# Performance work log

Measured on AMD Instinct MI355X. Metric: run time of the kernel, lower is better.

The kernel has to match this reference:

```python
import jax, jax.numpy as jnp
import numpy as np

INF = 100000000.0
TOPK = 13
ALPHA = 1
BETA = 6


def box_cxcywh_to_xyxy(b):
    cx, cy, w, h = jnp.split(b, 4, axis=-1)
    return jnp.concatenate([cx - 0.5 * w, cy - 0.5 * h, cx + 0.5 * w, cy + 0.5 * h], axis=-1)


def generalized_box_iou(boxes1, boxes2):
    # boxes1: [N,4] xyxy, boxes2: [G,4] xyxy -> [N,G]
    area1 = (boxes1[:, 2] - boxes1[:, 0]) * (boxes1[:, 3] - boxes1[:, 1])
    area2 = (boxes2[:, 2] - boxes2[:, 0]) * (boxes2[:, 3] - boxes2[:, 1])
    lt = jnp.maximum(boxes1[:, None, :2], boxes2[None, :, :2])
    rb = jnp.minimum(boxes1[:, None, 2:], boxes2[None, :, 2:])
    wh = jnp.clip(rb - lt, 0.0)
    inter = wh[..., 0] * wh[..., 1]
    union = area1[:, None] + area2[None, :] - inter
    iou = inter / union
    lt_e = jnp.minimum(boxes1[:, None, :2], boxes2[None, :, :2])
    rb_e = jnp.maximum(boxes1[:, None, 2:], boxes2[None, :, 2:])
    wh_e = jnp.clip(rb_e - lt_e, 0.0)
    area_e = wh_e[..., 0] * wh_e[..., 1]
    return iou - (area_e - union) / area_e


def _assign_one(cls_logits, bbox_pred, gt_boxes, gt_labels):
    # cls_logits [N,C], bbox_pred [N,4] cxcywh, gt_boxes [G,4] cxcywh, gt_labels [G]
    N = bbox_pred.shape[0]
    G = gt_boxes.shape[0]
    scores = jax.nn.sigmoid(cls_logits)
    overlaps = -generalized_box_iou(box_cxcywh_to_xyxy(bbox_pred), box_cxcywh_to_xyxy(gt_boxes))  # [N,G]
    bbox_scores = scores[:, gt_labels]                       # [N,G] gather per-gt class score
    alignment = bbox_scores ** ALPHA * overlaps ** BETA      # [N,G]
    # per-gt topk over queries
    cand_metrics, cand_idxs = jax.lax.top_k(alignment.T, TOPK)  # [G,K]
    is_pos = cand_metrics > 0
    vals = jnp.take_along_axis(overlaps.T, cand_idxs, axis=1)   # [G,K]
    rows = jnp.broadcast_to(jnp.arange(G)[:, None], (G, TOPK))
    cols = jnp.where(is_pos, cand_idxs, N)  # out-of-bounds col -> dropped
    oinf = jnp.full((G, N), -INF, dtype=overlaps.dtype)
    oinf = oinf.at[rows, cols].set(vals, mode='drop')
    max_overlaps = oinf.max(axis=0)     # [N]
    argmax_overlaps = oinf.argmax(axis=0)
    pos = max_overlaps != -INF
    assigned_gt_inds = jnp.where(pos, argmax_overlaps + 1, 0)
    assign_metrics = jnp.where(pos, alignment[jnp.arange(N), argmax_overlaps], 0.0)
    assigned_labels = jnp.where(pos, gt_labels[argmax_overlaps], -1)
    return assigned_gt_inds, assigned_labels, assign_metrics


def setup_inputs() -> dict:
    key = jax.random.key(0)
    k1, k2, k3, k4 = jax.random.split(key, 4)
    bs, N, C, G = 16, 4000, 80, 300
    return {
        'pred_logits': jax.random.normal(k1, (bs, N, C), dtype=jnp.float32),
        'pred_boxes': jax.random.uniform(k2, (bs, N, 4), dtype=jnp.float32, minval=0.05, maxval=0.95),
        'gt_boxes': jax.random.uniform(k3, (bs, G, 4), dtype=jnp.float32, minval=0.05, maxval=0.95),
        'gt_labels': jax.random.randint(k4, (bs, G), 0, C),
    }


def reference(pred_logits, pred_boxes, gt_boxes, gt_labels):
    # Fixed-shape equivalent of matched_list: assigned_gt_inds[b,q] == 0 means
    # background; k>0 means query q matched to gt k-1 (same semantics as the
    # (valid_query_idx, valid_assigned_gt_inds) pairs in the torch code).
    return jax.vmap(_assign_one)(pred_logits, pred_boxes, gt_boxes, gt_labels)
```

## Files before the change

### kernel.cpp

```cpp
#include <hip/hip_runtime.h>

#define NPRED  4000
#define NGROUP 1000
#define NGT    300
#define NCLS   80
#define TOPKK  13
#define NCHUNK 125

typedef unsigned long long u64;

__device__ __forceinline__ float frcp(float x) { return __builtin_amdgcn_rcpf(x); }
__device__ __forceinline__ float fexp(float x) {
    return __builtin_amdgcn_exp2f(x * 1.44269504088896341f);
}

__device__ __forceinline__ float neg_giou_x(float4 p, float gx1, float gy1,
                                            float gx2, float gy2, float garea) {
    float pa  = (p.z - p.x) * (p.w - p.y);
    float whx = fmaxf(fminf(p.z, gx2) - fmaxf(p.x, gx1), 0.0f);
    float why = fmaxf(fminf(p.w, gy2) - fmaxf(p.y, gy1), 0.0f);
    float inter = whx * why;
    float uni = pa + garea - inter;
    float iou = inter * frcp(uni);
    float wex = fmaxf(p.z, gx2) - fminf(p.x, gx1);
    float wey = fmaxf(p.w, gy2) - fminf(p.y, gy1);
    float area_e = wex * wey;
    return (area_e - uni) * frcp(area_e) - iou;
}

__device__ __forceinline__ float4 to_xyxy(float4 pb) {
    return make_float4(pb.x - 0.5f * pb.z, pb.y - 0.5f * pb.w,
                       pb.x + 0.5f * pb.z, pb.y + 0.5f * pb.w);
}

__device__ __forceinline__ float sigmoid_fast(float x) {
    return frcp(1.0f + fexp(-x));
}

__device__ __forceinline__ float pow6(float x) {
    float x2 = x * x;
    float x4 = x2 * x2;
    return x2 * x4;
}

__device__ __forceinline__ unsigned ord_float(float f) {
    unsigned u = __float_as_uint(f);
    return u ^ ((unsigned)(((int)u) >> 31) | 0x80000000u);
}

__device__ __forceinline__ u64 pack_key(float v, int n) {
    return ((u64)__float_as_uint(v) << 32) | (u64)(~(unsigned)n);
}

__global__ void init_keys(u64* keys, int n) {
    int i = blockIdx.x * blockDim.x + threadIdx.x;
    if (i < n) keys[i] = 0ULL;
}

__global__ __launch_bounds__(256) void sig_transpose(const float* __restrict__ logits,
                                                     const float4* __restrict__ pboxes,
                                                     float* __restrict__ st,
                                                     float4* __restrict__ pxyxy,
                                                     u64* __restrict__ keys,
                                                     int total_keys) {
    const int tid = threadIdx.x;
    const int gid = blockIdx.x * 256 + tid;
    if (gid < total_keys) keys[gid] = 0ULL;

    const int b = blockIdx.x / NCHUNK;
    const int n0 = (blockIdx.x % NCHUNK) * 32;

    if (tid < 32) {
        pxyxy[(size_t)b * NPRED + n0 + tid] =
            to_xyxy(pboxes[(size_t)b * NPRED + n0 + tid]);
    }

    __shared__ float tile[NCLS][32 + 1];

    const float4* src = (const float4*)(logits + ((size_t)b * NPRED + n0) * NCLS);
    #pragma unroll
    for (int it = 0; it < 3; ++it) {
        int i4 = tid + it * 256;
        if (i4 < 640) {
            int p = i4 / 20;
            int c = (i4 - p * 20) * 4;
            float4 v = src[i4];
            tile[c + 0][p] = sigmoid_fast(v.x);
            tile[c + 1][p] = sigmoid_fast(v.y);
            tile[c + 2][p] = sigmoid_fast(v.z);
            tile[c + 3][p] = sigmoid_fast(v.w);
        }
    }
    __syncthreads();
    float* dstbase = st + (size_t)b * NCLS * NPRED + n0;
    #pragma unroll
    for (int it = 0; it < 3; ++it) {
        int w4 = tid + it * 256;
        if (w4 < 640) {
            int c = w4 >> 3, r4 = (w4 & 7) * 4;
            float4 v = make_float4(tile[c][r4], tile[c][r4 + 1],
                                   tile[c][r4 + 2], tile[c][r4 + 3]);
            *(float4*)(dstbase + (size_t)c * NPRED + r4) = v;
        }
    }
}

template <bool PRE>
__global__ __launch_bounds__(256) void topk_scatter(const float* __restrict__ logits,
                                                    const float* __restrict__ st,
                                                    const float4* __restrict__ pboxes,
                                                    const float4* __restrict__ pxyxy,
                                                    const float4* __restrict__ gboxes,
                                                    const int* __restrict__ glabels,
                                                    u64* __restrict__ keys) {
    const int blk = blockIdx.x;
    const int b = blk / NGT;
    const int g = blk - b * NGT;
    const int tid = threadIdx.x;
    const int wave = tid >> 6;
    const int lane = tid & 63;

    __shared__ __align__(16) float s_key[NPRED];
    __shared__ u64 s_wave[4];
    __shared__ u64 s_win[TOPKK];

    float4 gb = gboxes[b * NGT + g];
    const int lab = glabels[b * NGT + g];
    const float gx1 = gb.x - 0.5f * gb.z;
    const float gy1 = gb.y - 0.5f * gb.w;
    const float gx2 = gb.x + 0.5f * gb.z;
    const float gy2 = gb.y + 0.5f * gb.w;
    const float garea = (gx2 - gx1) * (gy2 - gy1);

    const float* lg = logits + (size_t)b * NPRED * NCLS + lab;
    const float* srow = st + ((size_t)b * NCLS + lab) * NPRED;
    const float4* srow4 = (const float4*)srow;
    const float4* pbb = pboxes + (size_t)b * NPRED;
    const float4* pxr = pxyxy + (size_t)b * NPRED;

    u64 b1 = 0ULL, b2 = 0ULL;
    #pragma unroll
    for (int j = 0; j < 4; ++j) {
        int grp = tid + j * 256;
        if (grp < NGROUP) {
            int n0 = grp * 4;
            float s0, s1, s2, s3;
            float4 p0, p1, p2, p3;
            if (PRE) {
                float4 s4 = srow4[grp];
                s0 = s4.x; s1 = s4.y; s2 = s4.z; s3 = s4.w;
                p0 = pxr[n0]; p1 = pxr[n0 + 1]; p2 = pxr[n0 + 2]; p3 = pxr[n0 + 3];
            } else {
                s0 = sigmoid_fast(lg[(size_t)(n0 + 0) * NCLS]);
                s1 = sigmoid_fast(lg[(size_t)(n0 + 1) * NCLS]);
                s2 = sigmoid_fast(lg[(size_t)(n0 + 2) * NCLS]);
                s3 = sigmoid_fast(lg[(size_t)(n0 + 3) * NCLS]);
                p0 = to_xyxy(pbb[n0]);     p1 = to_xyxy(pbb[n0 + 1]);
                p2 = to_xyxy(pbb[n0 + 2]); p3 = to_xyxy(pbb[n0 + 3]);
            }
            float v0 = s0 * pow6(neg_giou_x(p0, gx1, gy1, gx2, gy2, garea));
            float v1 = s1 * pow6(neg_giou_x(p1, gx1, gy1, gx2, gy2, garea));
            float v2 = s2 * pow6(neg_giou_x(p2, gx1, gy1, gx2, gy2, garea));
            float v3 = s3 * pow6(neg_giou_x(p3, gx1, gy1, gx2, gy2, garea));
            *(float4*)&s_key[n0] = make_float4(v0, v1, v2, v3);
            u64 k0 = pack_key(v0, n0);
            u64 k1 = pack_key(v1, n0 + 1);
            u64 k2 = pack_key(v2, n0 + 2);
            u64 k3 = pack_key(v3, n0 + 3);
            if (k0 > b1) { b2 = b1; b1 = k0; } else if (k0 > b2) b2 = k0;
            if (k1 > b1) { b2 = b1; b1 = k1; } else if (k1 > b2) b2 = k1;
            if (k2 > b1) { b2 = b1; b1 = k2; } else if (k2 > b2) b2 = k2;
            if (k3 > b1) { b2 = b1; b1 = k3; } else if (k3 > b2) b2 = k3;
        }
    }

    {
        u64 m1 = b1;
        #pragma unroll
        for (int m = 1; m < 64; m <<= 1) {
            u64 o = __shfl_xor(m1, m, 64);
            if (o > m1) m1 = o;
        }
        if (lane == 0) s_wave[wave] = m1;
    }

    int nwin = 0;
    for (int k = 0; k < TOPKK; ++k) {
        __syncthreads();
        u64 t1 = s_wave[0];
        u64 c;
        c = s_wave[1]; if (c > t1) t1 = c;
        c = s_wave[2]; if (c > t1) t1 = c;
        c = s_wave[3]; if (c > t1) t1 = c;
        if ((unsigned)(t1 >> 32) == 0u) break;
        if (tid == 0) s_win[k] = t1;
        nwin = k + 1;
        int n1 = (int)(~(unsigned)t1);
        int ownerTid = (n1 >> 2) & 255;
        if (tid == ownerTid) {
            s_key[n1] = 0.0f;
            if (b2 != 0ULL) { b1 = b2; b2 = 0ULL; }
            else {
                b1 = 0ULL;
                #pragma unroll
                for (int jj = 0; jj < 4; ++jj) {
                    int grp = tid + jj * 256;
                    if (grp >= NGROUP) continue;
                    int n0 = grp * 4;
                    float4 q = *(const float4*)&s_key[n0];
                    u64 c0 = pack_key(q.x, n0);
                    u64 c1 = pack_key(q.y, n0 + 1);
                    u64 c2 = pack_key(q.z, n0 + 2);
                    u64 c3 = pack_key(q.w, n0 + 3);
                    if (c0 > b1) { b2 = b1; b1 = c0; } else if (c0 > b2) b2 = c0;
                    if (c1 > b1) { b2 = b1; b1 = c1; } else if (c1 > b2) b2 = c1;
                    if (c2 > b1) { b2 = b1; b1 = c2; } else if (c2 > b2) b2 = c2;
                    if (c3 > b1) { b2 = b1; b1 = c3; } else if (c3 > b2) b2 = c3;
                }
            }
        }
        if ((ownerTid >> 6) == wave) {
            u64 m1 = b1;
            #pragma unroll
            for (int m = 1; m < 64; m <<= 1) {
                u64 o = __shfl_xor(m1, m, 64);
                if (o > m1) m1 = o;
            }
            if (lane == 0) s_wave[wave] = m1;
        }
    }
    __syncthreads();

    if (tid < nwin) {
        u64 t = s_win[tid];
        int wi = (int)(~(unsigned)t);
        float o;
        if (PRE) {
            o = neg_giou_x(pxr[wi], gx1, gy1, gx2, gy2, garea);
        } else {
            o = neg_giou_x(to_xyxy(pbb[wi]), gx1, gy1, gx2, gy2, garea);
        }
        unsigned mbits = (unsigned)(t >> 32) >> 16;
        u64 key = ((u64)ord_float(o) << 32)
                | ((u64)(511u - (unsigned)g) << 23)
                | ((u64)mbits << 7);
        atomicMax(&keys[(size_t)b * NPRED + wi], key);
    }
}

__global__ void finalize(const int* __restrict__ glabels,
                         const u64* __restrict__ keys,
                         float* __restrict__ out, int total) {
    int i = blockIdx.x * blockDim.x + threadIdx.x;
    if (i >= total) return;
    int b = i / NPRED;
    u64 key = keys[i];
    float o0 = 0.0f, o1 = -1.0f, o2 = 0.0f;
    if (key != 0ULL) {
        int g = 511 - (int)((key >> 23) & 0x1FF);
        o0 = (float)(g + 1);
        o1 = (float)glabels[b * NGT + g];
        o2 = __uint_as_float(((unsigned)(key >> 7) & 0xFFFFu) << 16);
    }
    out[i] = o0;
    out[(size_t)total + i] = o1;
    out[(size_t)2 * total + i] = o2;
}

extern "C" void kernel_launch(void* const* d_in, const int* in_sizes, int n_in,
                              void* d_out, int out_size, void* d_ws, size_t ws_size,
                              hipStream_t stream) {
    const float* logits  = (const float*)d_in[0];
    const float4* pboxes = (const float4*)d_in[1];
    const float4* gboxes = (const float4*)d_in[2];
    const int* glabels   = (const int*)d_in[3];

    const int bs = in_sizes[3] / NGT;
    const int total = bs * NPRED;
    char* ws = (char*)d_ws;
    u64* keys   = (u64*)ws;                    ws += (size_t)total * 8;
    float* st   = (float*)ws;                  ws += (size_t)bs * NCLS * NPRED * 4;
    float4* pxy = (float4*)ws;                 ws += (size_t)total * 16;
    float* out = (float*)d_out;

    const size_t need = (size_t)(ws - (char*)d_ws);
    if (ws_size >= need) {
        sig_transpose<<<bs * NCHUNK, 256, 0, stream>>>(logits, pboxes, st, pxy,
                                                       keys, total);
        topk_scatter<true><<<bs * NGT, 256, 0, stream>>>(logits, st, pboxes, pxy,
                                                         gboxes, glabels, keys);
    } else {
        init_keys<<<(total + 255) / 256, 256, 0, stream>>>(keys, total);
        topk_scatter<false><<<bs * NGT, 256, 0, stream>>>(logits, st, pboxes, pxy,
                                                          gboxes, glabels, keys);
    }
    finalize<<<(total + 255) / 256, 256, 0, stream>>>(glabels, keys, out, total);
}
```

Baseline: 124.1 us.

## Run top-k extraction in a single wave without block barriers; precompute pred areas

The 13-step top-k selection loop no longer uses a __syncthreads per step across four waves. Each thread writes its top-2 candidates to shared memory, and wave 0 alone iterates, with each lane owning four threads' candidate pairs. Winners are held in lane registers for the final scatter, and three waves exit early. Predicted box areas are also computed once in the preprocessing kernel and loaded as float4, which adds a workspace buffer and extra global reads in exchange for fewer ALU ops per pair.

```diff
diff --git a/kernel.cpp b/kernel.cpp
--- a/kernel.cpp
+++ b/kernel.cpp
@@ -14,9 +14,8 @@
     return __builtin_amdgcn_exp2f(x * 1.44269504088896341f);
 }
 
-__device__ __forceinline__ float neg_giou_x(float4 p, float gx1, float gy1,
-                                            float gx2, float gy2, float garea) {
-    float pa  = (p.z - p.x) * (p.w - p.y);
+__device__ __forceinline__ float neg_giou_pa(float4 p, float pa, float gx1, float gy1,
+                                             float gx2, float gy2, float garea) {
     float whx = fmaxf(fminf(p.z, gx2) - fmaxf(p.x, gx1), 0.0f);
     float why = fmaxf(fminf(p.w, gy2) - fmaxf(p.y, gy1), 0.0f);
     float inter = whx * why;
@@ -52,6 +51,29 @@
     return ((u64)__float_as_uint(v) << 32) | (u64)(~(unsigned)n);
 }
 
+__device__ __forceinline__ u64 umax64(u64 a, u64 b) { return a > b ? a : b; }
+
+__device__ __forceinline__ void top2_insert(u64 k, u64& b1, u64& b2) {
+    if (k > b1) { b2 = b1; b1 = k; } else if (k > b2) b2 = k;
+}
+
+__device__ __forceinline__ void rescan_thread(const float* s_key, int t,
+                                              u64& r1, u64& r2) {
+    r1 = 0ULL; r2 = 0ULL;
+    #pragma unroll
+    for (int j = 0; j < 4; ++j) {
+        int grp = t + j * 256;
+        if (grp < NGROUP) {
+            int n0 = grp * 4;
+            float4 q = *(const float4*)&s_key[n0];
+            top2_insert(pack_key(q.x, n0),     r1, r2);
+            top2_insert(pack_key(q.y, n0 + 1), r1, r2);
+            top2_insert(pack_key(q.z, n0 + 2), r1, r2);
+            top2_insert(pack_key(q.w, n0 + 3), r1, r2);
+        }
+    }
+}
+
 __global__ void init_keys(u64* keys, int n) {
     int i = blockIdx.x * blockDim.x + threadIdx.x;
     if (i < n) keys[i] = 0ULL;
@@ -61,6 +83,7 @@
                                                      const float4* __restrict__ pboxes,
                                                      float* __restrict__ st,
                                                      float4* __restrict__ pxyxy,
+                                                     float* __restrict__ parea,
                                                      u64* __restrict__ keys,
                                                      int total_keys) {
     const int tid = threadIdx.x;
@@ -71,8 +94,10 @@
     const int n0 = (blockIdx.x % NCHUNK) * 32;
 
     if (tid < 32) {
-        pxyxy[(size_t)b * NPRED + n0 + tid] =
-            to_xyxy(pboxes[(size_t)b * NPRED + n0 + tid]);
+        int n = n0 + tid;
+        float4 x = to_xyxy(pboxes[(size_t)b * NPRED + n]);
+        pxyxy[(size_t)b * NPRED + n] = x;
+        parea[(size_t)b * NPRED + n] = (x.z - x.x) * (x.w - x.y);
     }
 
     __shared__ float tile[NCLS][32 + 1];
@@ -110,6 +135,7 @@
                                                     const float* __restrict__ st,
                                                     const float4* __restrict__ pboxes,
                                                     const float4* __restrict__ pxyxy,
+                                                    const float* __restrict__ parea,
                                                     const float4* __restrict__ gboxes,
                                                     const int* __restrict__ glabels,
                                                     u64* __restrict__ keys) {
@@ -121,8 +147,8 @@
     const int lane = tid & 63;
 
     __shared__ __align__(16) float s_key[NPRED];
-    __shared__ u64 s_wave[4];
-    __shared__ u64 s_win[TOPKK];
+    __shared__ __align__(16) u64 s_top1[256];
+    __shared__ __align__(16) u64 s_top2[256];
 
     float4 gb = gboxes[b * NGT + g];
     const int lab = glabels[b * NGT + g];
@@ -133,8 +159,8 @@
     const float garea = (gx2 - gx1) * (gy2 - gy1);
 
     const float* lg = logits + (size_t)b * NPRED * NCLS + lab;
-    const float* srow = st + ((size_t)b * NCLS + lab) * NPRED;
-    const float4* srow4 = (const float4*)srow;
+    const float4* srow4 = (const float4*)(st + ((size_t)b * NCLS + lab) * NPRED);
+    const float4* par4  = (const float4*)(parea + (size_t)b * NPRED);
     const float4* pbb = pboxes + (size_t)b * NPRED;
     const float4* pxr = pxyxy + (size_t)b * NPRED;
 
@@ -146,9 +172,12 @@
             int n0 = grp * 4;
             float s0, s1, s2, s3;
             float4 p0, p1, p2, p3;
+            float a0, a1, a2, a3;
             if (PRE) {
                 float4 s4 = srow4[grp];
                 s0 = s4.x; s1 = s4.y; s2 = s4.z; s3 = s4.w;
+                float4 a4 = par4[grp];
+                a0 = a4.x; a1 = a4.y; a2 = a4.z; a3 = a4.w;
                 p0 = pxr[n0]; p1 = pxr[n0 + 1]; p2 = pxr[n0 + 2]; p3 = pxr[n0 + 3];
             } else {
                 s0 = sigmoid_fast(lg[(size_t)(n0 + 0) * NCLS]);
@@ -157,89 +186,65 @@
                 s3 = sigmoid_fast(lg[(size_t)(n0 + 3) * NCLS]);
                 p0 = to_xyxy(pbb[n0]);     p1 = to_xyxy(pbb[n0 + 1]);
                 p2 = to_xyxy(pbb[n0 + 2]); p3 = to_xyxy(pbb[n0 + 3]);
+                a0 = (p0.z - p0.x) * (p0.w - p0.y);
+                a1 = (p1.z - p1.x) * (p1.w - p1.y);
+                a2 = (p2.z - p2.x) * (p2.w - p2.y);
+                a3 = (p3.z - p3.x) * (p3.w - p3.y);
             }
-            float v0 = s0 * pow6(neg_giou_x(p0, gx1, gy1, gx2, gy2, garea));
-            float v1 = s1 * pow6(neg_giou_x(p1, gx1, gy1, gx2, gy2, garea));
-            float v2 = s2 * pow6(neg_giou_x(p2, gx1, gy1, gx2, gy2, garea));
-            float v3 = s3 * pow6(neg_giou_x(p3, gx1, gy1, gx2, gy2, garea));
+            float v0 = s0 * pow6(neg_giou_pa(p0, a0, gx1, gy1, gx2, gy2, garea));
+            float v1 = s1 * pow6(neg_giou_pa(p1, a1, gx1, gy1, gx2, gy2, garea));
+            float v2 = s2 * pow6(neg_giou_pa(p2, a2, gx1, gy1, gx2, gy2, garea));
+            float v3 = s3 * pow6(neg_giou_pa(p3, a3, gx1, gy1, gx2, gy2, garea));
             *(float4*)&s_key[n0] = make_float4(v0, v1, v2, v3);
-            u64 k0 = pack_key(v0, n0);
-            u64 k1 = pack_key(v1, n0 + 1);
-            u64 k2 = pack_key(v2, n0 + 2);
-            u64 k3 = pack_key(v3, n0 + 3);
-            if (k0 > b1) { b2 = b1; b1 = k0; } else if (k0 > b2) b2 = k0;
-            if (k1 > b1) { b2 = b1; b1 = k1; } else if (k1 > b2) b2 = k1;
-            if (k2 > b1) { b2 = b1; b1 = k2; } else if (k2 > b2) b2 = k2;
-            if (k3 > b1) { b2 = b1; b1 = k3; } else if (k3 > b2) b2 = k3;
-        }
-    }
-
-    {
-        u64 m1 = b1;
-        #pragma unroll
-        for (int m = 1; m < 64; m <<= 1) {
-            u64 o = __shfl_xor(m1, m, 64);
-            if (o > m1) m1 = o;
-        }
-        if (lane == 0) s_wave[wave] = m1;
-    }
-
+            top2_insert(pack_key(v0, n0),     b1, b2);
+            top2_insert(pack_key(v1, n0 + 1), b1, b2);
+            top2_insert(pack_key(v2, n0 + 2), b1, b2);
+            top2_insert(pack_key(v3, n0 + 3), b1, b2);
+        }
+    }
+    s_top1[tid] = b1;
+    s_top2[tid] = b2;
+    __syncthreads();
+    if (wave != 0) return;
+
+    const int t0 = lane << 2;
+    u64 c0 = s_top1[t0 + 0], c1 = s_top1[t0 + 1],
+        c2 = s_top1[t0 + 2], c3 = s_top1[t0 + 3];
+    u64 d0 = s_top2[t0 + 0], d1 = s_top2[t0 + 1],
+        d2 = s_top2[t0 + 2], d3 = s_top2[t0 + 3];
+    u64 m = umax64(umax64(c0, c1), umax64(c2, c3));
+    u64 mywin = 0ULL;
     int nwin = 0;
     for (int k = 0; k < TOPKK; ++k) {
-        __syncthreads();
-        u64 t1 = s_wave[0];
-        u64 c;
-        c = s_wave[1]; if (c > t1) t1 = c;
-        c = s_wave[2]; if (c > t1) t1 = c;
-        c = s_wave[3]; if (c > t1) t1 = c;
-        if ((unsigned)(t1 >> 32) == 0u) break;
-        if (tid == 0) s_win[k] = t1;
-        nwin = k + 1;
-        int n1 = (int)(~(unsigned)t1);
-        int ownerTid = (n1 >> 2) & 255;
-        if (tid == ownerTid) {
+        u64 w = m;
+        #pragma unroll
+        for (int s = 1; s < 64; s <<= 1) {
+            u64 o = __shfl_xor(w, s, 64);
+            if (o > w) w = o;
+        }
+        if ((unsigned)(w >> 32) == 0u) break;
+        if (lane == k) mywin = w;
+        ++nwin;
+        bool h0 = (c0 == w), h1 = (c1 == w), h2 = (c2 == w), h3 = (c3 == w);
+        if (h0 | h1 | h2 | h3) {
+            int n1 = (int)(~(unsigned)w);
             s_key[n1] = 0.0f;
-            if (b2 != 0ULL) { b1 = b2; b2 = 0ULL; }
-            else {
-                b1 = 0ULL;
-                #pragma unroll
-                for (int jj = 0; jj < 4; ++jj) {
-                    int grp = tid + jj * 256;
-                    if (grp >= NGROUP) continue;
-                    int n0 = grp * 4;
-                    float4 q = *(const float4*)&s_key[n0];
-                    u64 c0 = pack_key(q.x, n0);
-                    u64 c1 = pack_key(q.y, n0 + 1);
-                    u64 c2 = pack_key(q.z, n0 + 2);
-                    u64 c3 = pack_key(q.w, n0 + 3);
-                    if (c0 > b1) { b2 = b1; b1 = c0; } else if (c0 > b2) b2 = c0;
-                    if (c1 > b1) { b2 = b1; b1 = c1; } else if (c1 > b2) b2 = c1;
-                    if (c2 > b1) { b2 = b1; b1 = c2; } else if (c2 > b2) b2 = c2;
-                    if (c3 > b1) { b2 = b1; b1 = c3; } else if (c3 > b2) b2 = c3;
-                }
-            }
-        }
-        if ((ownerTid >> 6) == wave) {
-            u64 m1 = b1;
-            #pragma unroll
-            for (int m = 1; m < 64; m <<= 1) {
-                u64 o = __shfl_xor(m1, m, 64);
-                if (o > m1) m1 = o;
-            }
-            if (lane == 0) s_wave[wave] = m1;
-        }
-    }
-    __syncthreads();
-
-    if (tid < nwin) {
-        u64 t = s_win[tid];
+            if (h0) { c0 = d0; d0 = 0ULL; if (c0 == 0ULL) rescan_thread(s_key, t0 + 0, c0, d0); }
+            if (h1) { c1 = d1; d1 = 0ULL; if (c1 == 0ULL) rescan_thread(s_key, t0 + 1, c1, d1); }
+            if (h2) { c2 = d2; d2 = 0ULL; if (c2 == 0ULL) rescan_thread(s_key, t0 + 2, c2, d2); }
+            if (h3) { c3 = d3; d3 = 0ULL; if (c3 == 0ULL) rescan_thread(s_key, t0 + 3, c3, d3); }
+            m = umax64(umax64(c0, c1), umax64(c2, c3));
+        }
+    }
+
+    if (lane < nwin) {
+        u64 t = mywin;
         int wi = (int)(~(unsigned)t);
-        float o;
-        if (PRE) {
-            o = neg_giou_x(pxr[wi], gx1, gy1, gx2, gy2, garea);
-        } else {
-            o = neg_giou_x(to_xyxy(pbb[wi]), gx1, gy1, gx2, gy2, garea);
-        }
+        float4 p;
+        if (PRE) p = pxr[wi];
+        else     p = to_xyxy(pbb[wi]);
+        float pa = (p.z - p.x) * (p.w - p.y);
+        float o = neg_giou_pa(p, pa, gx1, gy1, gx2, gy2, garea);
         unsigned mbits = (unsigned)(t >> 32) >> 16;
         u64 key = ((u64)ord_float(o) << 32)
                 | ((u64)(511u - (unsigned)g) << 23)
@@ -281,18 +286,19 @@
     u64* keys   = (u64*)ws;                    ws += (size_t)total * 8;
     float* st   = (float*)ws;                  ws += (size_t)bs * NCLS * NPRED * 4;
     float4* pxy = (float4*)ws;                 ws += (size_t)total * 16;
+    float* par  = (float*)ws;                  ws += (size_t)total * 4;
     float* out = (float*)d_out;
 
     const size_t need = (size_t)(ws - (char*)d_ws);
     if (ws_size >= need) {
         sig_transpose<<<bs * NCHUNK, 256, 0, stream>>>(logits, pboxes, st, pxy,
-                                                       keys, total);
+                                                       par, keys, total);
         topk_scatter<true><<<bs * NGT, 256, 0, stream>>>(logits, st, pboxes, pxy,
-                                                         gboxes, glabels, keys);
+                                                         par, gboxes, glabels, keys);
     } else {
         init_keys<<<(total + 255) / 256, 256, 0, stream>>>(keys, total);
         topk_scatter<false><<<bs * NGT, 256, 0, stream>>>(logits, st, pboxes, pxy,
-                                                          gboxes, glabels, keys);
+                                                          par, gboxes, glabels, keys);
     }
     finalize<<<(total + 255) / 256, 256, 0, stream>>>(glabels, keys, out, total);
 }
```

New measurement: 216.4 us. 1.74x slower.
